# Kernel optimization log

Measured on AMD Instinct MI355X. Metric: run time of the kernel, lower is better.

The kernel has to match this reference:

```python
import jax, jax.numpy as jnp
import numpy as np

N_NODES = 50000
IN_C, HID_C, OUT_C = 128, 128, 64
N_EDGES = 800000


def setup_inputs() -> dict:
    key = jax.random.key(0)
    k1, k2, k3, k4, k5, k6 = jax.random.split(key, 6)
    x = jax.random.normal(k1, (N_NODES, IN_C), dtype=jnp.float32)
    edge_index = jax.random.randint(k2, (2, N_EDGES), 0, N_NODES, dtype=jnp.int64)
    # Glorot-ish init for the two GCN layer weights + biases
    W1 = jax.random.normal(k3, (IN_C, HID_C), dtype=jnp.float32) / np.sqrt(IN_C)
    b1 = jnp.zeros((HID_C,), dtype=jnp.float32)
    W2 = jax.random.normal(k4, (HID_C, OUT_C), dtype=jnp.float32) / np.sqrt(HID_C)
    b2 = jnp.zeros((OUT_C,), dtype=jnp.float32)
    return {"x": x, "edge_index": edge_index, "W1": W1, "b1": b1, "W2": W2, "b2": b2}


def _gcn_norm(edge_index, num_nodes):
    # Add self-loops, then symmetric normalization: deg^-1/2[row] * deg^-1/2[col]
    loops = jnp.arange(num_nodes, dtype=edge_index.dtype)
    row = jnp.concatenate([edge_index[0], loops])  # target nodes
    col = jnp.concatenate([edge_index[1], loops])  # source nodes
    ones = jnp.ones(row.shape[0], dtype=jnp.float32)
    deg = jax.ops.segment_sum(ones, row, num_segments=num_nodes)
    dinv = jnp.where(deg > 0, jax.lax.rsqrt(jnp.maximum(deg, 1.0)), 0.0)
    norm = dinv[row] * dinv[col]  # [E + N]
    return row, col, norm


def _gcn_conv(x, row, col, norm, W, b, num_nodes):
    h = x @ W                              # [N, C_out] — transform first (fewer FLOPs)
    msg = h[col] * norm[:, None]           # gather + scale  [E+N, C_out]
    out = jax.ops.segment_sum(msg, row, num_segments=num_nodes)  # scatter-add
    return out + b


def reference(x, edge_index, W1, b1, W2, b2):
    n = x.shape[0]
    row, col, norm = _gcn_norm(edge_index, n)
    h = _gcn_conv(x, row, col, norm, W1, b1, n)
    # original applies x.relu() then non_linearity (ReLU()) — idempotent, one relu suffices
    h = jax.nn.relu(h)
    return _gcn_conv(h, row, col, norm, W2, b2, n)
```

## Files before the change

### kernel.cpp

```cpp
#include <hip/hip_runtime.h>


#define CHUNKS 256

typedef short bf16x8 __attribute__((ext_vector_type(8)));
typedef float f32x4 __attribute__((ext_vector_type(4)));

__device__ __forceinline__ float bf2f(unsigned int u16) {
    return __uint_as_float(u16 << 16);
}
__device__ __forceinline__ unsigned int f2bf_rne(float f) {
    unsigned int u = __float_as_uint(f);
    return (u + 0x7fffu + ((u >> 16) & 1u)) >> 16;
}
__device__ __forceinline__ unsigned int pack2bf(float a, float b) {
    return f2bf_rne(a) | (f2bf_rne(b) << 16);
}
__device__ __forceinline__ void add8(float* acc, uint4 p) {
    acc[0] += bf2f(p.x & 0xffffu); acc[1] += bf2f(p.x >> 16);
    acc[2] += bf2f(p.y & 0xffffu); acc[3] += bf2f(p.y >> 16);
    acc[4] += bf2f(p.z & 0xffffu); acc[5] += bf2f(p.z >> 16);
    acc[6] += bf2f(p.w & 0xffffu); acc[7] += bf2f(p.w >> 16);
}


__global__ __launch_bounds__(256) void hist_kernel(
    const int* __restrict__ row, int E, int CE, int NB, int* __restrict__ cnt)
{
    __shared__ int hist[256];
    const int c = blockIdx.x, t = threadIdx.x;
    hist[t] = 0;
    __syncthreads();
    int s = c * CE, e = min(E, s + CE);
    for (int i = s + t; i < e; i += 256) atomicAdd(&hist[row[i] >> 8], 1);
    __syncthreads();
    if (t < NB) cnt[t * CHUNKS + c] = hist[t];
}

__global__ __launch_bounds__(256) void scanA_kernel(int* __restrict__ cnt, int* __restrict__ tot)
{
    __shared__ int s[256];
    const int b = blockIdx.x, t = threadIdx.x;
    int v = cnt[b * CHUNKS + t];
    s[t] = v; __syncthreads();
    #pragma unroll
    for (int d = 1; d < 256; d <<= 1) {
        int xv = (t >= d) ? s[t - d] : 0;
        __syncthreads();
        s[t] += xv;
        __syncthreads();
    }
    cnt[b * CHUNKS + t] = s[t] - v;
    if (t == 255) tot[b] = s[255];
}

__global__ __launch_bounds__(256) void scanB_kernel(
    const int* __restrict__ tot, int* __restrict__ bstart, int NB, int E)
{
    __shared__ int s[256];
    const int t = threadIdx.x;
    int v = (t < NB) ? tot[t] : 0;
    s[t] = v; __syncthreads();
    #pragma unroll
    for (int d = 1; d < 256; d <<= 1) {
        int xv = (t >= d) ? s[t - d] : 0;
        __syncthreads();
        s[t] += xv;
        __syncthreads();
    }
    if (t < NB) bstart[t] = s[t] - v;
    if (t == 0) bstart[NB] = E;
}

__global__ __launch_bounds__(256) void scatter_kernel(
    const int* __restrict__ row, const int* __restrict__ col, int E, int CE, int NB,
    const int* __restrict__ cnt, const int* __restrict__ bstart,
    unsigned int* __restrict__ bucket)
{
    __shared__ int curL[256];
    const int c = blockIdx.x, t = threadIdx.x;
    if (t < NB) curL[t] = bstart[t] + cnt[t * CHUNKS + c];
    __syncthreads();
    int s = c * CE, e = min(E, s + CE);
    for (int i = s + t; i < e; i += 256) {
        int r = row[i];
        int b = r >> 8;
        int pos = atomicAdd(&curL[b], 1);
        bucket[pos] = (unsigned)(r & 255) | ((unsigned)col[i] << 8);
    }
}

__global__ __launch_bounds__(256) void bucketize_kernel(
    const int* __restrict__ bstart, unsigned int* __restrict__ bucket,
    float* __restrict__ dinv, int2* __restrict__ off2, int N)
{
    __shared__ unsigned int ent[8192];
    __shared__ int hist[256], scn[256], cnt2[256];
    const int b = blockIdx.x, t = threadIdx.x;
    const int n0 = b * 256;

    hist[t] = 0;
    cnt2[t] = 0;
    __syncthreads();

    const int bs = bstart[b], be = bstart[b + 1];
    const int m = min(be - bs, 8192);

    for (int i = t; i < m; i += 256) {
        unsigned int v = bucket[bs + i];
        ent[i] = v;
        atomicAdd(&hist[v & 255u], 1);
    }
    __syncthreads();

    int h = hist[t];
    scn[t] = h;
    __syncthreads();
    #pragma unroll
    for (int d = 1; d < 256; d <<= 1) {
        int xv = (t >= d) ? scn[t - d] : 0;
        __syncthreads();
        scn[t] += xv;
        __syncthreads();
    }
    int base = scn[t] - h;

    int node = n0 + t;
    if (node < N) {
        dinv[node] = rsqrtf((float)(h + 1));
        off2[node] = make_int2(bs + base, bs + base + h);
    }
    scn[t] = base;
    __syncthreads();

    for (int i = t; i < m; i += 256) {
        unsigned int v = ent[i];
        int r = v & 255u;
        int slot = atomicAdd(&cnt2[r], 1);
        bucket[bs + scn[r] + slot] = v >> 8;
    }
}


__global__ __launch_bounds__(256) void wtrans_kernel(
    const float* __restrict__ W1, const float* __restrict__ W2,
    unsigned short* __restrict__ Wt1, unsigned short* __restrict__ Wt2)
{
    int i = blockIdx.x * 256 + threadIdx.x;
    if (i < 128 * 128) {
        int k = i >> 7, c = i & 127;
        Wt1[c * 128 + k] = (unsigned short)f2bf_rne(W1[i]);
    } else {
        int j = i - 128 * 128;
        if (j < 128 * 64) {
            int k = j >> 6, c = j & 63;
            Wt2[c * 128 + k] = (unsigned short)f2bf_rne(W2[j]);
        }
    }
}

template <int CT, bool BF16IN>
__global__ __launch_bounds__(256) void gemm_mfma_kernel(
    const void* __restrict__ Xv, const unsigned short* __restrict__ Wt,
    const float* __restrict__ dinv, unsigned short* __restrict__ out, int N)
{
    constexpr int COUT = CT * 64;
    __shared__ unsigned short As[64 * 128];
    __shared__ unsigned short Bs[COUT * 128];
    __shared__ float dl[64];

    const int t = threadIdx.x;
    const int m0 = blockIdx.x * 64;

    if (BF16IN) {
        const unsigned short* X = (const unsigned short*)Xv;
        #pragma unroll
        for (int i = 0; i < 4; ++i) {
            int f = i * 256 + t;
            int r = f >> 4, c16 = f & 15;
            int rg = m0 + r;
            uint4 p = (rg < N) ? ((const uint4*)X)[(size_t)rg * 16 + c16]
                               : make_uint4(0u, 0u, 0u, 0u);
            int cb = c16 * 16;
            *(uint4*)((char*)As + r * 256 + (cb ^ ((r & 7) << 4))) = p;
        }
    } else {
        const float* X = (const float*)Xv;
        #pragma unroll
        for (int i = 0; i < 8; ++i) {
            int f = i * 256 + t;
            int r = f >> 5, c4 = f & 31;
            int rg = m0 + r;
            float4 v = (rg < N) ? ((const float4*)X)[(size_t)rg * 32 + c4]
                                : make_float4(0.f, 0.f, 0.f, 0.f);
            uint2 p;
            p.x = pack2bf(v.x, v.y);
            p.y = pack2bf(v.z, v.w);
            int cb = c4 * 8;
            *(uint2*)((char*)As + r * 256 + (cb ^ ((r & 7) << 4))) = p;
        }
    }
    #pragma unroll
    for (int i = 0; i < CT * 8; ++i) {
        int f = i * 256 + t;
        int r = f >> 5;
        int cb = (f & 31) * 8;
        uint2 p = ((const uint2*)Wt)[f];
        *(uint2*)((char*)Bs + r * 256 + (cb ^ ((r & 7) << 4))) = p;
    }
    if (t < 64) dl[t] = (m0 + t < N) ? dinv[m0 + t] : 0.f;
    __syncthreads();

    const int w = t >> 6, l = t & 63;
    const int lr = l & 15, lk = l >> 4;

    bf16x8 af[4][4];
    #pragma unroll
    for (int mt = 0; mt < 4; ++mt)
        #pragma unroll
        for (int kt = 0; kt < 4; ++kt) {
            int r = mt * 16 + lr;
            int cb = kt * 64 + lk * 16;
            af[mt][kt] = *(const bf16x8*)((const char*)As + r * 256 + (cb ^ ((r & 7) << 4)));
        }
    bf16x8 bfr[CT][4];
    #pragma unroll
    for (int ct = 0; ct < CT; ++ct)
        #pragma unroll
        for (int kt = 0; kt < 4; ++kt) {
            int c = w * (CT * 16) + ct * 16 + lr;
            int cb = kt * 64 + lk * 16;
            bfr[ct][kt] = *(const bf16x8*)((const char*)Bs + c * 256 + (cb ^ ((c & 7) << 4)));
        }

    f32x4 acc[4][CT];
    #pragma unroll
    for (int mt = 0; mt < 4; ++mt)
        #pragma unroll
        for (int ct = 0; ct < CT; ++ct)
            acc[mt][ct] = f32x4{0.f, 0.f, 0.f, 0.f};

    #pragma unroll
    for (int kt = 0; kt < 4; ++kt)
        #pragma unroll
        for (int mt = 0; mt < 4; ++mt)
            #pragma unroll
            for (int ct = 0; ct < CT; ++ct)
                acc[mt][ct] = __builtin_amdgcn_mfma_f32_16x16x32_bf16(
                    af[mt][kt], bfr[ct][kt], acc[mt][ct], 0, 0, 0);

    #pragma unroll
    for (int mt = 0; mt < 4; ++mt) {
        #pragma unroll
        for (int ct = 0; ct < CT; ++ct) {
            #pragma unroll
            for (int r = 0; r < 4; ++r) {
                int rowl = mt * 16 + lk * 4 + r;
                int grow = m0 + rowl;
                if (grow < N) {
                    int c = w * (CT * 16) + ct * 16 + lr;
                    float v = acc[mt][ct][r] * dl[rowl];
                    out[(size_t)grow * COUT + c] = (unsigned short)f2bf_rne(v);
                }
            }
        }
    }
}


__global__ __launch_bounds__(64) void agg1_kernel(
    const unsigned short* __restrict__ hs, const unsigned int* __restrict__ csr,
    const int2* __restrict__ off2, const float* __restrict__ dinv,
    const float* __restrict__ bias, unsigned short* __restrict__ out, int N)
{
    const int n = blockIdx.x;
    const int l = threadIdx.x;
    const int q = l & 15, g = l >> 4;

    float acc[8] = {};
    if (g == 0)
        add8(acc, *(const uint4*)&hs[(size_t)n * 128 + q * 8]);

    int2 se = off2[n];
    int j = se.x, e = se.y;
    for (; j + 7 < e; j += 8) {
        int c0 = csr[j + g], c1 = csr[j + 4 + g];
        uint4 p0 = *(const uint4*)&hs[(size_t)c0 * 128 + q * 8];
        uint4 p1 = *(const uint4*)&hs[(size_t)c1 * 128 + q * 8];
        add8(acc, p0);
        add8(acc, p1);
    }
    if (j + 3 < e) {
        add8(acc, *(const uint4*)&hs[(size_t)csr[j + g] * 128 + q * 8]);
        j += 4;
    }
    if (g < e - j)
        add8(acc, *(const uint4*)&hs[(size_t)csr[j + g] * 128 + q * 8]);

    #pragma unroll
    for (int i = 0; i < 8; ++i) {
        acc[i] += __shfl_xor(acc[i], 16);
        acc[i] += __shfl_xor(acc[i], 32);
    }

    if (g == 0) {
        float d = dinv[n];
        float4 b0 = ((const float4*)bias)[q * 2];
        float4 b1 = ((const float4*)bias)[q * 2 + 1];
        float v0 = fmaxf(d * acc[0] + b0.x, 0.f), v1 = fmaxf(d * acc[1] + b0.y, 0.f);
        float v2 = fmaxf(d * acc[2] + b0.z, 0.f), v3 = fmaxf(d * acc[3] + b0.w, 0.f);
        float v4 = fmaxf(d * acc[4] + b1.x, 0.f), v5 = fmaxf(d * acc[5] + b1.y, 0.f);
        float v6 = fmaxf(d * acc[6] + b1.z, 0.f), v7 = fmaxf(d * acc[7] + b1.w, 0.f);
        uint4 o;
        o.x = pack2bf(v0, v1); o.y = pack2bf(v2, v3);
        o.z = pack2bf(v4, v5); o.w = pack2bf(v6, v7);
        *(uint4*)&out[(size_t)n * 128 + q * 8] = o;
    }
}

__global__ __launch_bounds__(64) void agg2_kernel(
    const unsigned short* __restrict__ hs, const unsigned int* __restrict__ csr,
    const int2* __restrict__ off2, const float* __restrict__ dinv,
    const float* __restrict__ bias, float* __restrict__ out, int N)
{
    const int n = blockIdx.x;
    const int l = threadIdx.x;
    const int q = l & 7, g = l >> 3;

    float acc[8] = {};
    if (g == 0)
        add8(acc, *(const uint4*)&hs[(size_t)n * 64 + q * 8]);

    int2 se = off2[n];
    int j = se.x, e = se.y;
    for (; j + 15 < e; j += 16) {
        int c0 = csr[j + g], c1 = csr[j + 8 + g];
        uint4 p0 = *(const uint4*)&hs[(size_t)c0 * 64 + q * 8];
        uint4 p1 = *(const uint4*)&hs[(size_t)c1 * 64 + q * 8];
        add8(acc, p0);
        add8(acc, p1);
    }
    if (j + 7 < e) {
        add8(acc, *(const uint4*)&hs[(size_t)csr[j + g] * 64 + q * 8]);
        j += 8;
    }
    if (g < e - j)
        add8(acc, *(const uint4*)&hs[(size_t)csr[j + g] * 64 + q * 8]);

    #pragma unroll
    for (int i = 0; i < 8; ++i) {
        acc[i] += __shfl_xor(acc[i], 8);
        acc[i] += __shfl_xor(acc[i], 16);
        acc[i] += __shfl_xor(acc[i], 32);
    }

    if (g == 0) {
        float d = dinv[n];
        float4 b0 = ((const float4*)bias)[q * 2];
        float4 b1 = ((const float4*)bias)[q * 2 + 1];
        float4 o0, o1;
        o0.x = d * acc[0] + b0.x; o0.y = d * acc[1] + b0.y;
        o0.z = d * acc[2] + b0.z; o0.w = d * acc[3] + b0.w;
        o1.x = d * acc[4] + b1.x; o1.y = d * acc[5] + b1.y;
        o1.z = d * acc[6] + b1.z; o1.w = d * acc[7] + b1.w;
        *(float4*)&out[(size_t)n * 64 + q * 8] = o0;
        *(float4*)&out[(size_t)n * 64 + q * 8 + 4] = o1;
    }
}

extern "C" void kernel_launch(void* const* d_in, const int* in_sizes, int n_in,
                              void* d_out, int out_size, void* d_ws, size_t ws_size,
                              hipStream_t stream)
{
    const float* x  = (const float*)d_in[0];
    const int*   ei = (const int*)d_in[1];
    const float* W1 = (const float*)d_in[2];
    const float* b1 = (const float*)d_in[3];
    const float* W2 = (const float*)d_in[4];
    const float* b2 = (const float*)d_in[5];
    float* out = (float*)d_out;

    const int N = in_sizes[0] / 128;
    const int E = in_sizes[1] / 2;
    const int* row = ei;
    const int* col = ei + E;
    const int NB = (N + 255) / 256;
    const int CE = (E + CHUNKS - 1) / CHUNKS;

    char* ws = (char*)d_ws;
    size_t o = 0;
    auto take = [&](size_t bytes) { void* p = ws + o; o = (o + bytes + 255) & ~(size_t)255; return p; };
    int*   cnt    = (int*)  take((size_t)NB * CHUNKS * 4);
    int*   tot    = (int*)  take((size_t)NB * 4);
    int*   bstart = (int*)  take((size_t)(NB + 1) * 4);
    unsigned int* bucket = (unsigned int*)take((size_t)E * 4);
    float* dinv   = (float*)take((size_t)N * 4);
    int2*  off2   = (int2*) take((size_t)N * 8);
    unsigned short* Wt1 = (unsigned short*)take(128 * 128 * 2);
    unsigned short* Wt2 = (unsigned short*)take(64 * 128 * 2);
    unsigned short* hs  = (unsigned short*)take((size_t)N * 128 * 2);
    unsigned short* a1  = (unsigned short*)take((size_t)N * 128 * 2);
    unsigned short* hs2 = hs;

    hist_kernel<<<CHUNKS, 256, 0, stream>>>(row, E, CE, NB, cnt);
    scanA_kernel<<<NB, 256, 0, stream>>>(cnt, tot);
    scanB_kernel<<<1, 256, 0, stream>>>(tot, bstart, NB, E);
    scatter_kernel<<<CHUNKS, 256, 0, stream>>>(row, col, E, CE, NB, cnt, bstart, bucket);
    bucketize_kernel<<<NB, 256, 0, stream>>>(bstart, bucket, dinv, off2, N);

    wtrans_kernel<<<(128 * 128 + 128 * 64 + 255) / 256, 256, 0, stream>>>(W1, W2, Wt1, Wt2);

    gemm_mfma_kernel<2, false><<<(N + 63) / 64, 256, 0, stream>>>(x, Wt1, dinv, hs, N);
    agg1_kernel<<<N, 64, 0, stream>>>(hs, bucket, off2, dinv, b1, a1, N);

    gemm_mfma_kernel<1, true><<<(N + 63) / 64, 256, 0, stream>>>(a1, Wt2, dinv, hs2, N);
    agg2_kernel<<<N, 64, 0, stream>>>(hs2, bucket, off2, dinv, b2, out, N);
}
```

Measured before the change: 114.1 us.

## Fuse CSR build stages into one cooperative kernel and pack node metadata

Merges the histogram, two scans, scatter, bucketize and weight transpose kernels into a single cooperative kernel separated by grid-wide syncs, removing five kernel launches and their gaps. The aggregation kernels now handle four nodes per 256-thread block instead of one node per 64-thread block, and read offsets plus dinv from one packed int4 per node, with a simpler tail loop. Grid syncs add their own cost, and the cooperative launch needs all 256 blocks to be co-resident.

```diff
diff --git a/kernel.cpp b/kernel.cpp
--- a/kernel.cpp
+++ b/kernel.cpp
@@ -1,4 +1,7 @@
 #include <hip/hip_runtime.h>
+#include <hip/hip_cooperative_groups.h>
+
+namespace cg = cooperative_groups;
 
 
 #define CHUNKS 256
@@ -24,140 +27,120 @@
 }
 
 
-__global__ __launch_bounds__(256) void hist_kernel(
-    const int* __restrict__ row, int E, int CE, int NB, int* __restrict__ cnt)
+__global__ __launch_bounds__(256) void build_kernel(
+    const int* __restrict__ row, const int* __restrict__ col, int E, int CE, int NB,
+    const float* __restrict__ W1, const float* __restrict__ W2,
+    unsigned short* __restrict__ Wt1, unsigned short* __restrict__ Wt2,
+    int* __restrict__ cnt, int* __restrict__ tot, int* __restrict__ bstart,
+    unsigned int* __restrict__ bucket, float* __restrict__ dinv,
+    int4* __restrict__ nod, int N)
 {
-    __shared__ int hist[256];
-    const int c = blockIdx.x, t = threadIdx.x;
-    hist[t] = 0;
+    cg::grid_group grid = cg::this_grid();
+    __shared__ unsigned int ent[8192];
+    __shared__ int sA[256], sB[256], sC[256];
+    const int b = blockIdx.x, t = threadIdx.x;
+
+    sA[t] = 0;
     __syncthreads();
-    int s = c * CE, e = min(E, s + CE);
-    for (int i = s + t; i < e; i += 256) atomicAdd(&hist[row[i] >> 8], 1);
-    __syncthreads();
-    if (t < NB) cnt[t * CHUNKS + c] = hist[t];
-}
-
-__global__ __launch_bounds__(256) void scanA_kernel(int* __restrict__ cnt, int* __restrict__ tot)
-{
-    __shared__ int s[256];
-    const int b = blockIdx.x, t = threadIdx.x;
-    int v = cnt[b * CHUNKS + t];
-    s[t] = v; __syncthreads();
-    #pragma unroll
-    for (int d = 1; d < 256; d <<= 1) {
-        int xv = (t >= d) ? s[t - d] : 0;
-        __syncthreads();
-        s[t] += xv;
-        __syncthreads();
-    }
-    cnt[b * CHUNKS + t] = s[t] - v;
-    if (t == 255) tot[b] = s[255];
-}
-
-__global__ __launch_bounds__(256) void scanB_kernel(
-    const int* __restrict__ tot, int* __restrict__ bstart, int NB, int E)
-{
-    __shared__ int s[256];
-    const int t = threadIdx.x;
-    int v = (t < NB) ? tot[t] : 0;
-    s[t] = v; __syncthreads();
-    #pragma unroll
-    for (int d = 1; d < 256; d <<= 1) {
-        int xv = (t >= d) ? s[t - d] : 0;
-        __syncthreads();
-        s[t] += xv;
-        __syncthreads();
-    }
-    if (t < NB) bstart[t] = s[t] - v;
-    if (t == 0) bstart[NB] = E;
-}
-
-__global__ __launch_bounds__(256) void scatter_kernel(
-    const int* __restrict__ row, const int* __restrict__ col, int E, int CE, int NB,
-    const int* __restrict__ cnt, const int* __restrict__ bstart,
-    unsigned int* __restrict__ bucket)
-{
-    __shared__ int curL[256];
-    const int c = blockIdx.x, t = threadIdx.x;
-    if (t < NB) curL[t] = bstart[t] + cnt[t * CHUNKS + c];
-    __syncthreads();
-    int s = c * CE, e = min(E, s + CE);
-    for (int i = s + t; i < e; i += 256) {
-        int r = row[i];
-        int b = r >> 8;
-        int pos = atomicAdd(&curL[b], 1);
-        bucket[pos] = (unsigned)(r & 255) | ((unsigned)col[i] << 8);
-    }
-}
-
-__global__ __launch_bounds__(256) void bucketize_kernel(
-    const int* __restrict__ bstart, unsigned int* __restrict__ bucket,
-    float* __restrict__ dinv, int2* __restrict__ off2, int N)
-{
-    __shared__ unsigned int ent[8192];
-    __shared__ int hist[256], scn[256], cnt2[256];
-    const int b = blockIdx.x, t = threadIdx.x;
-    const int n0 = b * 256;
-
-    hist[t] = 0;
-    cnt2[t] = 0;
-    __syncthreads();
-
-    const int bs = bstart[b], be = bstart[b + 1];
-    const int m = min(be - bs, 8192);
-
-    for (int i = t; i < m; i += 256) {
-        unsigned int v = bucket[bs + i];
-        ent[i] = v;
-        atomicAdd(&hist[v & 255u], 1);
-    }
-    __syncthreads();
-
-    int h = hist[t];
-    scn[t] = h;
-    __syncthreads();
-    #pragma unroll
-    for (int d = 1; d < 256; d <<= 1) {
-        int xv = (t >= d) ? scn[t - d] : 0;
-        __syncthreads();
-        scn[t] += xv;
-        __syncthreads();
-    }
-    int base = scn[t] - h;
-
-    int node = n0 + t;
-    if (node < N) {
-        dinv[node] = rsqrtf((float)(h + 1));
-        off2[node] = make_int2(bs + base, bs + base + h);
-    }
-    scn[t] = base;
-    __syncthreads();
-
-    for (int i = t; i < m; i += 256) {
-        unsigned int v = ent[i];
-        int r = v & 255u;
-        int slot = atomicAdd(&cnt2[r], 1);
-        bucket[bs + scn[r] + slot] = v >> 8;
-    }
-}
-
-
-__global__ __launch_bounds__(256) void wtrans_kernel(
-    const float* __restrict__ W1, const float* __restrict__ W2,
-    unsigned short* __restrict__ Wt1, unsigned short* __restrict__ Wt2)
-{
-    int i = blockIdx.x * 256 + threadIdx.x;
-    if (i < 128 * 128) {
-        int k = i >> 7, c = i & 127;
-        Wt1[c * 128 + k] = (unsigned short)f2bf_rne(W1[i]);
-    } else {
-        int j = i - 128 * 128;
-        if (j < 128 * 64) {
+    {
+        int s = b * CE, e = min(E, s + CE);
+        for (int i = s + t; i < e; i += 256) atomicAdd(&sA[row[i] >> 8], 1);
+        int i = b * 256 + t;
+        if (i < 128 * 128) {
+            int k = i >> 7, c = i & 127;
+            Wt1[c * 128 + k] = (unsigned short)f2bf_rne(W1[i]);
+        } else if (i < 128 * 128 + 128 * 64) {
+            int j = i - 128 * 128;
             int k = j >> 6, c = j & 63;
             Wt2[c * 128 + k] = (unsigned short)f2bf_rne(W2[j]);
         }
-    }
-}
+        __syncthreads();
+        if (t < NB) cnt[t * CHUNKS + b] = sA[t];
+    }
+    grid.sync();
+
+    if (b < NB) {
+        int v = cnt[b * CHUNKS + t];
+        sB[t] = v; __syncthreads();
+        #pragma unroll
+        for (int d = 1; d < 256; d <<= 1) {
+            int xv = (t >= d) ? sB[t - d] : 0;
+            __syncthreads();
+            sB[t] += xv;
+            __syncthreads();
+        }
+        cnt[b * CHUNKS + t] = sB[t] - v;
+        if (t == 255) tot[b] = sB[255];
+    }
+    grid.sync();
+
+    if (b == 0) {
+        int v = (t < NB) ? tot[t] : 0;
+        sC[t] = v; __syncthreads();
+        #pragma unroll
+        for (int d = 1; d < 256; d <<= 1) {
+            int xv = (t >= d) ? sC[t - d] : 0;
+            __syncthreads();
+            sC[t] += xv;
+            __syncthreads();
+        }
+        if (t < NB) bstart[t] = sC[t] - v;
+        if (t == 0) bstart[NB] = E;
+    }
+    grid.sync();
+
+    {
+        if (t < NB) sA[t] = bstart[t] + cnt[t * CHUNKS + b];
+        __syncthreads();
+        int s = b * CE, e = min(E, s + CE);
+        for (int i = s + t; i < e; i += 256) {
+            int r = row[i];
+            int pos = atomicAdd(&sA[r >> 8], 1);
+            bucket[pos] = (unsigned)(r & 255) | ((unsigned)col[i] << 8);
+        }
+    }
+    grid.sync();
+
+    if (b < NB) {
+        sA[t] = 0;
+        sC[t] = 0;
+        __syncthreads();
+        const int bs = bstart[b], be = bstart[b + 1];
+        const int m = min(be - bs, 8192);
+        for (int i = t; i < m; i += 256) {
+            unsigned int v = bucket[bs + i];
+            ent[i] = v;
+            atomicAdd(&sA[v & 255u], 1);
+        }
+        __syncthreads();
+        int h = sA[t];
+        sB[t] = h;
+        __syncthreads();
+        #pragma unroll
+        for (int d = 1; d < 256; d <<= 1) {
+            int xv = (t >= d) ? sB[t - d] : 0;
+            __syncthreads();
+            sB[t] += xv;
+            __syncthreads();
+        }
+        int base = sB[t] - h;
+        int node = b * 256 + t;
+        if (node < N) {
+            float dv = rsqrtf((float)(h + 1));
+            dinv[node] = dv;
+            nod[node] = make_int4(bs + base, bs + base + h, __float_as_int(dv), 0);
+        }
+        sB[t] = base;
+        __syncthreads();
+        for (int i = t; i < m; i += 256) {
+            unsigned int v = ent[i];
+            int r = v & 255u;
+            int slot = atomicAdd(&sC[r], 1);
+            bucket[bs + sB[r] + slot] = v >> 8;
+        }
+    }
+}
+
 
 template <int CT, bool BF16IN>
 __global__ __launch_bounds__(256) void gemm_mfma_kernel(
@@ -268,34 +251,32 @@
 }
 
 
-__global__ __launch_bounds__(64) void agg1_kernel(
+__global__ __launch_bounds__(256) void agg1_kernel(
     const unsigned short* __restrict__ hs, const unsigned int* __restrict__ csr,
-    const int2* __restrict__ off2, const float* __restrict__ dinv,
-    const float* __restrict__ bias, unsigned short* __restrict__ out, int N)
+    const int4* __restrict__ nod, const float* __restrict__ bias,
+    unsigned short* __restrict__ out, int N)
 {
-    const int n = blockIdx.x;
-    const int l = threadIdx.x;
+    const int w = threadIdx.x >> 6, l = threadIdx.x & 63;
+    const int n = blockIdx.x * 4 + w;
+    if (n >= N) return;
     const int q = l & 15, g = l >> 4;
 
+    int4 se = nod[n];
     float acc[8] = {};
     if (g == 0)
         add8(acc, *(const uint4*)&hs[(size_t)n * 128 + q * 8]);
 
-    int2 se = off2[n];
-    int j = se.x, e = se.y;
-    for (; j + 7 < e; j += 8) {
-        int c0 = csr[j + g], c1 = csr[j + 4 + g];
+    int j = se.x + g;
+    const int e = se.y;
+    for (; j + 4 < e; j += 8) {
+        int c0 = csr[j], c1 = csr[j + 4];
         uint4 p0 = *(const uint4*)&hs[(size_t)c0 * 128 + q * 8];
         uint4 p1 = *(const uint4*)&hs[(size_t)c1 * 128 + q * 8];
         add8(acc, p0);
         add8(acc, p1);
     }
-    if (j + 3 < e) {
-        add8(acc, *(const uint4*)&hs[(size_t)csr[j + g] * 128 + q * 8]);
-        j += 4;
-    }
-    if (g < e - j)
-        add8(acc, *(const uint4*)&hs[(size_t)csr[j + g] * 128 + q * 8]);
+    if (j < e)
+        add8(acc, *(const uint4*)&hs[(size_t)csr[j] * 128 + q * 8]);
 
     #pragma unroll
     for (int i = 0; i < 8; ++i) {
@@ -304,7 +285,7 @@
     }
 
     if (g == 0) {
-        float d = dinv[n];
+        float d = __int_as_float(se.z);
         float4 b0 = ((const float4*)bias)[q * 2];
         float4 b1 = ((const float4*)bias)[q * 2 + 1];
         float v0 = fmaxf(d * acc[0] + b0.x, 0.f), v1 = fmaxf(d * acc[1] + b0.y, 0.f);
@@ -318,34 +299,32 @@
     }
 }
 
-__global__ __launch_bounds__(64) void agg2_kernel(
+__global__ __launch_bounds__(256) void agg2_kernel(
     const unsigned short* __restrict__ hs, const unsigned int* __restrict__ csr,
-    const int2* __restrict__ off2, const float* __restrict__ dinv,
-    const float* __restrict__ bias, float* __restrict__ out, int N)
+    const int4* __restrict__ nod, const float* __restrict__ bias,
+    float* __restrict__ out, int N)
 {
-    const int n = blockIdx.x;
-    const int l = threadIdx.x;
+    const int w = threadIdx.x >> 6, l = threadIdx.x & 63;
+    const int n = blockIdx.x * 4 + w;
+    if (n >= N) return;
     const int q = l & 7, g = l >> 3;
 
+    int4 se = nod[n];
     float acc[8] = {};
     if (g == 0)
         add8(acc, *(const uint4*)&hs[(size_t)n * 64 + q * 8]);
 
-    int2 se = off2[n];
-    int j = se.x, e = se.y;
-    for (; j + 15 < e; j += 16) {
-        int c0 = csr[j + g], c1 = csr[j + 8 + g];
+    int j = se.x + g;
+    const int e = se.y;
+    for (; j + 8 < e; j += 16) {
+        int c0 = csr[j], c1 = csr[j + 8];
         uint4 p0 = *(const uint4*)&hs[(size_t)c0 * 64 + q * 8];
         uint4 p1 = *(const uint4*)&hs[(size_t)c1 * 64 + q * 8];
         add8(acc, p0);
         add8(acc, p1);
     }
-    if (j + 7 < e) {
-        add8(acc, *(const uint4*)&hs[(size_t)csr[j + g] * 64 + q * 8]);
-        j += 8;
-    }
-    if (g < e - j)
-        add8(acc, *(const uint4*)&hs[(size_t)csr[j + g] * 64 + q * 8]);
+    if (j < e)
+        add8(acc, *(const uint4*)&hs[(size_t)csr[j] * 64 + q * 8]);
 
     #pragma unroll
     for (int i = 0; i < 8; ++i) {
@@ -355,7 +334,7 @@
     }
 
     if (g == 0) {
-        float d = dinv[n];
+        float d = __int_as_float(se.z);
         float4 b0 = ((const float4*)bias)[q * 2];
         float4 b1 = ((const float4*)bias)[q * 2 + 1];
         float4 o0, o1;
@@ -395,24 +374,28 @@
     int*   bstart = (int*)  take((size_t)(NB + 1) * 4);
     unsigned int* bucket = (unsigned int*)take((size_t)E * 4);
     float* dinv   = (float*)take((size_t)N * 4);
-    int2*  off2   = (int2*) take((size_t)N * 8);
+    int4*  nod    = (int4*) take((size_t)N * 16);
     unsigned short* Wt1 = (unsigned short*)take(128 * 128 * 2);
     unsigned short* Wt2 = (unsigned short*)take(64 * 128 * 2);
     unsigned short* hs  = (unsigned short*)take((size_t)N * 128 * 2);
     unsigned short* a1  = (unsigned short*)take((size_t)N * 128 * 2);
     unsigned short* hs2 = hs;
 
-    hist_kernel<<<CHUNKS, 256, 0, stream>>>(row, E, CE, NB, cnt);
-    scanA_kernel<<<NB, 256, 0, stream>>>(cnt, tot);
-    scanB_kernel<<<1, 256, 0, stream>>>(tot, bstart, NB, E);
-    scatter_kernel<<<CHUNKS, 256, 0, stream>>>(row, col, E, CE, NB, cnt, bstart, bucket);
-    bucketize_kernel<<<NB, 256, 0, stream>>>(bstart, bucket, dinv, off2, N);
-
-    wtrans_kernel<<<(128 * 128 + 128 * 64 + 255) / 256, 256, 0, stream>>>(W1, W2, Wt1, Wt2);
+    {
+        int E_ = E, CE_ = CE, NB_ = NB, N_ = N;
+        void* args[] = {
+            (void*)&row, (void*)&col, (void*)&E_, (void*)&CE_, (void*)&NB_,
+            (void*)&W1, (void*)&W2, (void*)&Wt1, (void*)&Wt2,
+            (void*)&cnt, (void*)&tot, (void*)&bstart,
+            (void*)&bucket, (void*)&dinv, (void*)&nod, (void*)&N_
+        };
+        hipLaunchCooperativeKernel((void*)build_kernel, dim3(CHUNKS), dim3(256),
+                                   args, 0, stream);
+    }
 
     gemm_mfma_kernel<2, false><<<(N + 63) / 64, 256, 0, stream>>>(x, Wt1, dinv, hs, N);
-    agg1_kernel<<<N, 64, 0, stream>>>(hs, bucket, off2, dinv, b1, a1, N);
+    agg1_kernel<<<(N + 3) / 4, 256, 0, stream>>>(hs, bucket, nod, b1, a1, N);
 
     gemm_mfma_kernel<1, true><<<(N + 63) / 64, 256, 0, stream>>>(a1, Wt2, dinv, hs2, N);
-    agg2_kernel<<<N, 64, 0, stream>>>(hs2, bucket, off2, dinv, b2, out, N);
-}
+    agg2_kernel<<<(N + 3) / 4, 256, 0, stream>>>(hs2, bucket, nod, b2, out, N);
+}
```

Measured after the change: 241.7 us. 112% more time.
